# Kernel optimization log

Hardware: AMD Instinct MI355X
Metric: run time of the kernel (lower is better)

The kernel has to match this reference:

```python
import jax, jax.numpy as jnp
import numpy as np

D = 768

def setup_inputs() -> dict:
    key = jax.random.key(0)
    ks = jax.random.split(key, 12)
    inp = {
        "text_embeddings": jax.random.normal(ks[0], (8, 512, D), dtype=jnp.float32),
        "kb_emb": jax.random.normal(ks[1], (200000, D), dtype=jnp.float32),
        "W_ret": jax.random.normal(ks[2], (D, D), dtype=jnp.float32) * 0.02,
        "b_ret": jax.random.normal(ks[3], (D,), dtype=jnp.float32) * 0.02,
        "Ws1": jax.random.normal(ks[4], (2 * D, D), dtype=jnp.float32) * 0.02,
        "bs1": jax.random.normal(ks[5], (D,), dtype=jnp.float32) * 0.02,
        "Ws2": jax.random.normal(ks[6], (D, 1), dtype=jnp.float32) * 0.02,
        "bs2": jax.random.normal(ks[7], (1,), dtype=jnp.float32) * 0.02,
        "mention_sent": jax.random.randint(ks[8], (256,), 0, 8, dtype=jnp.int32),
        "mention_start": jax.random.randint(ks[9], (256,), 0, 480, dtype=jnp.int32),
        "mention_len": jax.random.randint(ks[10], (256,), 0, 31, dtype=jnp.int32),
        "top_k": 100,
    }
    return inp


def reference(text_embeddings, kb_emb, W_ret, b_ret, Ws1, bs1, Ws2, bs2,
              mention_sent, mention_start, mention_len, top_k):
    S = text_embeddings.shape[1]
    pos = jnp.arange(S, dtype=jnp.int32)
    # inclusive span [start, start+len] -> mask [M, S]
    mask = (pos[None, :] >= mention_start[:, None]) & (pos[None, :] <= (mention_start + mention_len)[:, None])
    maskf = mask.astype(text_embeddings.dtype)
    sent = text_embeddings[mention_sent]                       # [M, S, D]
    mention_emb = jnp.einsum('msd,ms->md', sent, maskf) / maskf.sum(1, keepdims=True)

    # entity_retriever linear, then KB dot-product retrieval of top 2k candidates
    query = mention_emb @ W_ret.T + b_ret                      # [M, D]
    sims = query @ kb_emb.T                                    # [M, N]
    _, cand_idx = jax.lax.top_k(sims, 2 * top_k)               # [M, 2k]
    cand_embs = kb_emb[cand_idx]                               # [M, 2k, D]

    # candidate_scorer: Linear(2D->D) on concat(mention, cand) + ReLU + Linear(D->1) + Sigmoid
    m_part = mention_emb @ Ws1[:D]                             # [M, D]
    c_part = jnp.einsum('mkd,de->mke', cand_embs, Ws1[D:])     # [M, 2k, D]
    h = jax.nn.relu(m_part[:, None, :] + c_part + bs1)
    scores = jax.nn.sigmoid(jnp.einsum('mke,eo->mko', h, Ws2)[..., 0] + bs2[0])  # [M, 2k]

    top_scores, ti = jax.lax.top_k(scores, top_k)              # [M, k]
    top_kb_idx = jnp.take_along_axis(cand_idx, ti, axis=1)
    return top_scores, top_kb_idx
```

## Files before the change

kernel.cpp:

```cpp
#include <hip/hip_runtime.h>
#include <cfloat>
#include <cmath>
#include <cstdint>

#define DD 768
#define MM 256
#define NKB 200000
#define SLEN 512
#define KK 200
#define TOPK 100
#define SURV_CAP 1024
#define RESC 232
#define THRC 2.70f
#define MAXMARK 32768
#define DELTA 4e-5
#define NET 12

typedef __attribute__((ext_vector_type(8))) short bf16x8;
typedef __attribute__((ext_vector_type(4))) float f32x4;

__device__ __forceinline__ unsigned short f2bf_rne(float x) {
  unsigned u = __float_as_uint(x);
  unsigned r = (u + 0x7FFFu + ((u >> 16) & 1u)) >> 16;
  return (unsigned short)r;
}
__device__ __forceinline__ float bf2f(unsigned short us) {
  return __uint_as_float(((unsigned)us) << 16);
}
__device__ __forceinline__ void splitbf(float x, unsigned short& hi, unsigned short& lo) {
  hi = f2bf_rne(x);
  lo = f2bf_rne(x - bf2f(hi));
}

__global__ __launch_bounds__(256) void k_prepT(
    const float* __restrict__ Wret, float* __restrict__ WretT) {
  __shared__ float tile[64][65];
  int e0 = blockIdx.x * 64, d0 = blockIdx.y * 64;
  int tid = threadIdx.x;
  int r = tid >> 6, cc = tid & 63;
  for (int i = 0; i < 64; i += 4)
    tile[r + i][cc] = Wret[(size_t)(e0 + r + i) * DD + d0 + cc];
  __syncthreads();
  for (int i = 0; i < 64; i += 4)
    WretT[(size_t)(d0 + r + i) * DD + e0 + cc] = tile[cc][r + i];
}

__global__ __launch_bounds__(256) void k_front(
    const float* __restrict__ text, const int* __restrict__ msent,
    const int* __restrict__ mstart, const int* __restrict__ mlen,
    const float* __restrict__ WretT, const float* __restrict__ bret,
    const float* __restrict__ Ws1,
    double* __restrict__ q64, unsigned short* __restrict__ qb16,
    float* __restrict__ tthr, double* __restrict__ mp64,
    float* __restrict__ mp32) {
  int m = blockIdx.x;
  __shared__ double sme[DD];
  __shared__ float snorm[256];
  int tid = threadIdx.x;
  {
    int sent = msent[m], st = mstart[m], ln = mlen[m];
    const float* base = text + (size_t)sent * SLEN * DD;
    for (int d = tid; d < DD; d += 256) {
      double acc = 0.0;
      for (int s = st; s <= st + ln; ++s) acc += (double)base[(size_t)s * DD + d];
      sme[d] = acc / (double)(ln + 1);
    }
  }
  __syncthreads();
  float nloc = 0.f;
  for (int e = tid; e < DD; e += 256) {
    double aq = (double)bret[e];
    double amp = 0.0;
    for (int d = 0; d < DD; ++d) {
      double md = sme[d];
      aq  += md * (double)WretT[(size_t)d * DD + e];
      amp += md * (double)Ws1[(size_t)d * DD + e];
    }
    q64[(size_t)m * DD + e] = aq;
    qb16[(size_t)m * DD + e] = f2bf_rne((float)aq);
    mp64[(size_t)m * DD + e] = amp;
    mp32[(size_t)m * DD + e] = (float)amp;
    nloc += (float)(aq * aq);
  }
  snorm[tid] = nloc; __syncthreads();
  for (int s = 128; s > 0; s >>= 1) {
    if (tid < s) snorm[tid] += snorm[tid + s];
    __syncthreads();
  }
  if (tid == 0) tthr[m] = THRC * sqrtf(snorm[0]);
}

__global__ __launch_bounds__(256) void k_prep(
    const float* __restrict__ Ws1, unsigned short* __restrict__ Bth,
    unsigned short* __restrict__ Btl) {
  int e = blockIdx.x;
  for (int k = threadIdx.x; k < DD; k += 256) {
    float x = Ws1[(size_t)(DD + k) * DD + e];
    unsigned short hi, lo;
    splitbf(x, hi, lo);
    Bth[(size_t)e * DD + k] = hi;
    Btl[(size_t)e * DD + k] = lo;
  }
}

__global__ __launch_bounds__(512) void k_sims_mfma(
    const unsigned short* __restrict__ qb, const float* __restrict__ kb,
    const float* __restrict__ tthr, int* __restrict__ gcnt,
    uint2* __restrict__ gcand) {
  __shared__ unsigned short Bs[64 * 32];
  __shared__ float sthr[256];
  int n0 = blockIdx.x * 64;
  int tid = threadIdx.x;
  int lane = tid & 63, w = tid >> 6;
  int h = lane >> 4, c = lane & 15;
  if (tid < 256) sthr[tid] = tthr[tid];
  f32x4 acc[2][4] = {};
  const int brow = n0 + (tid >> 3);
  const int bk4  = (tid & 7) * 4;
  const int bwoff = ((tid >> 3) * 64 + (tid & 7) * 8) ^ (((tid >> 3) & 7) << 4);
  auto ldB = [&](int k0, float4 &dst) {
    dst = *(const float4*)(kb + (size_t)brow * DD + k0 + bk4);
  };
  auto stB = [&](const float4 &v) {
    uint2 p;
    p.x = (unsigned)f2bf_rne(v.x) | ((unsigned)f2bf_rne(v.y) << 16);
    p.y = (unsigned)f2bf_rne(v.z) | ((unsigned)f2bf_rne(v.w) << 16);
    *(uint2*)((char*)Bs + bwoff) = p;
  };
  const unsigned short* qa0 = qb + (size_t)(w * 32 + c) * DD;
  const unsigned short* qa1 = qb + (size_t)(w * 32 + 16 + c) * DD;
  auto step = [&](int k0, float4 &cur, float4 &nxt, bool pf) {
    bf16x8 a0 = *(const bf16x8*)(qa0 + k0 + h * 8);
    bf16x8 a1 = *(const bf16x8*)(qa1 + k0 + h * 8);
    __syncthreads();
    stB(cur);
    if (pf) ldB(k0 + 32, nxt);
    __syncthreads();
#pragma unroll
    for (int nf = 0; nf < 4; ++nf) {
      int n = nf * 16 + c;
      int off = (n * 64 + h * 16) ^ ((n & 7) << 4);
      bf16x8 b = *(bf16x8*)((char*)Bs + off);
      acc[0][nf] = __builtin_amdgcn_mfma_f32_16x16x32_bf16(a0, b, acc[0][nf], 0, 0, 0);
      acc[1][nf] = __builtin_amdgcn_mfma_f32_16x16x32_bf16(a1, b, acc[1][nf], 0, 0, 0);
    }
  };
  float4 b0, b1;
  ldB(0, b0);
#pragma unroll
  for (int kc = 0; kc < 12; ++kc) {
    step(kc * 64,      b0, b1, true);
    step(kc * 64 + 32, b1, b0, kc < 11);
  }
#pragma unroll
  for (int mf = 0; mf < 2; ++mf)
#pragma unroll
    for (int nf = 0; nf < 4; ++nf)
#pragma unroll
      for (int r = 0; r < 4; ++r) {
        int row = w * 32 + mf * 16 + h * 4 + r;
        int col = n0 + nf * 16 + c;
        float v = acc[mf][nf][r];
        if (v > sthr[row]) {
          int p = atomicAdd(&gcnt[row], 1);
          if (p < SURV_CAP) gcand[(size_t)row * SURV_CAP + p] = make_uint2(__float_as_uint(v), (unsigned)col);
        }
      }
}

__global__ __launch_bounds__(256) void k_select(
    const uint2* __restrict__ gcand, const int* __restrict__ gcnt,
    const float* __restrict__ kb, const double* __restrict__ q64,
    int* __restrict__ cidx) {
  int m = blockIdx.x;
  __shared__ float skf[SURV_CAP];
  __shared__ int   sidx[SURV_CAP];
  __shared__ double sq[DD];
  __shared__ double skey[256];
  __shared__ int    skidx[256];
  int tid = threadIdx.x;
  int cnt = gcnt[m]; if (cnt > SURV_CAP) cnt = SURV_CAP;
  for (int d = tid; d < DD; d += 256) sq[d] = q64[(size_t)m * DD + d];
  for (int i = tid; i < SURV_CAP; i += 256) {
    if (i < cnt) {
      uint2 v = gcand[(size_t)m * SURV_CAP + i];
      skf[i] = __uint_as_float(v.x);
      sidx[i] = (int)v.y;
    } else { skf[i] = -FLT_MAX; sidx[i] = 0x7fffffff; }
  }
  __syncthreads();
  for (int k = 2; k <= SURV_CAP; k <<= 1) {
    for (int j = k >> 1; j > 0; j >>= 1) {
      for (int i = tid; i < SURV_CAP; i += 256) {
        int l = i ^ j;
        if (l > i) {
          float ka = skf[i], kb2 = skf[l];
          int ia = sidx[i], ib = sidx[l];
          bool lBefore = (kb2 > ka) || (kb2 == ka && ib < ia);
          bool iBefore = (ka > kb2) || (ka == kb2 && ia < ib);
          bool dir = ((i & k) == 0);
          bool sw = dir ? lBefore : iBefore;
          if (sw) { skf[i] = kb2; skf[l] = ka; sidx[i] = ib; sidx[l] = ia; }
        }
      }
      __syncthreads();
    }
  }
  int lane = tid & 63, wv = tid >> 6;
  for (int cpos = wv; cpos < RESC; cpos += 4) {
    int ci = sidx[cpos];
    double s;
    if (ci < NKB) {
      const float* krow = kb + (size_t)ci * DD;
      double acc = 0.0;
      for (int d = lane; d < DD; d += 64) acc += sq[d] * (double)krow[d];
      for (int off2 = 32; off2 > 0; off2 >>= 1) acc += __shfl_down(acc, off2, 64);
      s = acc;
    } else s = -INFINITY;
    if (lane == 0) { skey[cpos] = s; skidx[cpos] = ci; }
  }
  if (tid >= RESC && tid < 256) { skey[tid] = -INFINITY; skidx[tid] = 0x7fffffff; }
  __syncthreads();
  for (int k = 2; k <= 256; k <<= 1) {
    for (int j = k >> 1; j > 0; j >>= 1) {
      int i = tid, l = i ^ j;
      if (l > i) {
        double ka = skey[i], kb2 = skey[l];
        int ia = skidx[i], ib = skidx[l];
        bool lBefore = (kb2 > ka) || (kb2 == ka && ib < ia);
        bool iBefore = (ka > kb2) || (ka == kb2 && ia < ib);
        bool dir = ((i & k) == 0);
        bool sw = dir ? lBefore : iBefore;
        if (sw) { skey[i] = kb2; skey[l] = ka; skidx[i] = ib; skidx[l] = ia; }
      }
      __syncthreads();
    }
  }
  for (int cc = tid; cc < KK; cc += 256) {
    int v = skidx[cc];
    cidx[(size_t)m * KK + cc] = (v < NKB) ? v : 0;
  }
}

__global__ __launch_bounds__(256) void k_score2(
    const float* __restrict__ kb, const int* __restrict__ cidx,
    const float* __restrict__ mp32, const unsigned short* __restrict__ Bth,
    const unsigned short* __restrict__ Btl, const float* __restrict__ bs1,
    const float* __restrict__ Ws2, float* __restrict__ gpart) {
  __shared__ unsigned short Ah[256 * 32], Al[256 * 32];
  __shared__ unsigned short Bh[64 * 32], Bl[64 * 32];
  __shared__ float smp[3][64], sb1v[64], sw2v[64];
  __shared__ int srow[256];
  int p = blockIdx.x;
  int x = p & 7, j = p >> 3;
  int ct = x + 8 * (j / NET), et = j % NET;
  int r0 = ct * 256, e0 = et * 64;
  int tid = threadIdx.x, lane = tid & 63, w = tid >> 6;
  int h = lane >> 4, c = lane & 15;
  srow[tid] = cidx[r0 + tid];
  int m0 = r0 / KK;
  int mm1 = (m0 + 1 < MM) ? m0 + 1 : MM - 1;
  int mm2 = (m0 + 2 < MM) ? m0 + 2 : MM - 1;
  if (tid < 64) {
    smp[0][tid] = mp32[(size_t)m0 * DD + e0 + tid];
    smp[1][tid] = mp32[(size_t)mm1 * DD + e0 + tid];
    smp[2][tid] = mp32[(size_t)mm2 * DD + e0 + tid];
    sb1v[tid] = bs1[e0 + tid];
    sw2v[tid] = Ws2[e0 + tid];
  }
  __syncthreads();
  const float* aaddr[8];
#pragma unroll
  for (int it = 0; it < 8; ++it) {
    int idx = tid + it * 256;
    int rr = idx >> 3, f4 = idx & 7;
    aaddr[it] = kb + (size_t)srow[rr] * DD + f4 * 4;
  }
  const int be = tid >> 2, bk8 = tid & 3;
  const unsigned short* bhaddr = Bth + (size_t)(e0 + be) * DD + bk8 * 8;
  const unsigned short* bladdr = Btl + (size_t)(e0 + be) * DD + bk8 * 8;
  float4 pa[8];
  uint4 pbh, pbl;
#pragma unroll
  for (int it = 0; it < 8; ++it) pa[it] = *(const float4*)(aaddr[it]);
  pbh = *(const uint4*)(bhaddr);
  pbl = *(const uint4*)(bladdr);
  f32x4 acc[4][4] = {};
  for (int k0 = 0; k0 < DD; k0 += 32) {
    __syncthreads();
#pragma unroll
    for (int it = 0; it < 8; ++it) {
      int idx = tid + it * 256;
      int rr = idx >> 3, f4 = idx & 7;
      float4 v = pa[it];
      unsigned short h0, h1, h2, h3, l0, l1, l2, l3;
      splitbf(v.x, h0, l0); splitbf(v.y, h1, l1);
      splitbf(v.z, h2, l2); splitbf(v.w, h3, l3);
      uint2 ph, pl;
      ph.x = (unsigned)h0 | ((unsigned)h1 << 16); ph.y = (unsigned)h2 | ((unsigned)h3 << 16);
      pl.x = (unsigned)l0 | ((unsigned)l1 << 16); pl.y = (unsigned)l2 | ((unsigned)l3 << 16);
      int off = (rr * 64 + f4 * 8) ^ ((rr & 7) << 4);
      *(uint2*)((char*)Ah + off) = ph;
      *(uint2*)((char*)Al + off) = pl;
    }
    {
      int off = (be * 64 + bk8 * 16) ^ ((be & 7) << 4);
      *(uint4*)((char*)Bh + off) = pbh;
      *(uint4*)((char*)Bl + off) = pbl;
    }
    if (k0 + 32 < DD) {
#pragma unroll
      for (int it = 0; it < 8; ++it) pa[it] = *(const float4*)(aaddr[it] + k0 + 32);
      pbh = *(const uint4*)(bhaddr + k0 + 32);
      pbl = *(const uint4*)(bladdr + k0 + 32);
    }
    __syncthreads();
    bf16x8 ah[4], al[4];
#pragma unroll
    for (int mf = 0; mf < 4; ++mf) {
      int rr = w * 64 + mf * 16 + c;
      int off = (rr * 64 + h * 16) ^ ((rr & 7) << 4);
      ah[mf] = *(bf16x8*)((char*)Ah + off);
      al[mf] = *(bf16x8*)((char*)Al + off);
    }
#pragma unroll
    for (int nf = 0; nf < 4; ++nf) {
      int e = nf * 16 + c;
      int off = (e * 64 + h * 16) ^ ((e & 7) << 4);
      bf16x8 bh = *(bf16x8*)((char*)Bh + off);
      bf16x8 bl = *(bf16x8*)((char*)Bl + off);
#pragma unroll
      for (int mf = 0; mf < 4; ++mf) {
        acc[mf][nf] = __builtin_amdgcn_mfma_f32_16x16x32_bf16(ah[mf], bh, acc[mf][nf], 0, 0, 0);
        acc[mf][nf] = __builtin_amdgcn_mfma_f32_16x16x32_bf16(ah[mf], bl, acc[mf][nf], 0, 0, 0);
        acc[mf][nf] = __builtin_amdgcn_mfma_f32_16x16x32_bf16(al[mf], bh, acc[mf][nf], 0, 0, 0);
      }
    }
  }
  int bnd1 = (m0 + 1) * KK, bnd2 = (m0 + 2) * KK;
#pragma unroll
  for (int mf = 0; mf < 4; ++mf) {
    float zp[4] = {0.f, 0.f, 0.f, 0.f};
#pragma unroll
    for (int nf = 0; nf < 4; ++nf) {
      int el = nf * 16 + c;
      float b1v = sb1v[el], w2v = sw2v[el];
#pragma unroll
      for (int r = 0; r < 4; ++r) {
        int rowg = r0 + w * 64 + mf * 16 + h * 4 + r;
        int sel = (rowg >= bnd1) + (rowg >= bnd2);
        float hh = acc[mf][nf][r] + smp[sel][el] + b1v;
        if (hh > 0.f) zp[r] += hh * w2v;
      }
    }
#pragma unroll
    for (int r = 0; r < 4; ++r) {
      float v = zp[r];
      v += __shfl_xor(v, 1, 64);
      v += __shfl_xor(v, 2, 64);
      v += __shfl_xor(v, 4, 64);
      v += __shfl_xor(v, 8, 64);
      if (c == 0)
        gpart[(size_t)(r0 + w * 64 + mf * 16 + h * 4 + r) * NET + et] = v;
    }
  }
}

__global__ __launch_bounds__(256) void k_mark(
    const float* __restrict__ gpart, const float* __restrict__ bs2,
    double* __restrict__ z64, int* __restrict__ marks, int* __restrict__ mcnt) {
  int m = blockIdx.x;
  __shared__ double sk[256];
  __shared__ int sp[256];
  __shared__ int flag[256];
  int tid = threadIdx.x;
  flag[tid] = 0;
  if (tid < KK) {
    double s = 0.0;
#pragma unroll
    for (int i = 0; i < NET; ++i) s += (double)gpart[(size_t)(m * KK + tid) * NET + i];
    s += (double)bs2[0];
    z64[(size_t)m * KK + tid] = s;
    sk[tid] = s; sp[tid] = tid;
  } else { sk[tid] = -INFINITY; sp[tid] = 0x7fffffff; }
  __syncthreads();
  for (int k = 2; k <= 256; k <<= 1) {
    for (int j = k >> 1; j > 0; j >>= 1) {
      int i = tid, l = i ^ j;
      if (l > i) {
        double ka = sk[i], kb2 = sk[l];
        int ia = sp[i], ib = sp[l];
        bool lBefore = (kb2 > ka) || (kb2 == ka && ib < ia);
        bool iBefore = (ka > kb2) || (ka == kb2 && ia < ib);
        bool dir = ((i & k) == 0);
        bool sw = dir ? lBefore : iBefore;
        if (sw) { sk[i] = kb2; sk[l] = ka; sp[i] = ib; sp[l] = ia; }
      }
      __syncthreads();
    }
  }
  if (tid <= 120) {
    if (sk[tid] - sk[tid + 1] < DELTA) {
      flag[tid] = 1;
      atomicExch(&flag[tid + 1], 1);
    }
  }
  __syncthreads();
  if (tid <= 121 && flag[tid]) {
    int p = atomicAdd(mcnt, 1);
    if (p < MAXMARK) marks[p] = m * KK + sp[tid];
  }
}

__global__ __launch_bounds__(256) void k_rescore(
    const float* __restrict__ kb, const int* __restrict__ cidx,
    const double* __restrict__ mp64, const float* __restrict__ Ws1,
    const float* __restrict__ bs1, const float* __restrict__ Ws2,
    const float* __restrict__ bs2, const int* __restrict__ marks,
    const int* __restrict__ mcnt, double* __restrict__ z64) {
  int cnt = *mcnt; if (cnt > MAXMARK) cnt = MAXMARK;
  __shared__ float sc[DD];
  __shared__ double sred[256];
  int tid = threadIdx.x;
  for (int it = blockIdx.x; it < cnt; it += gridDim.x) {
    int r = marks[it];
    int m = r / KK;
    int row = cidx[r];
    for (int d = tid; d < DD; d += 256) sc[d] = kb[(size_t)row * DD + d];
    __syncthreads();
    double pz = 0.0;
    for (int e = tid; e < DD; e += 256) {
      double a = 0.0;
      for (int d = 0; d < DD; ++d) a += (double)sc[d] * (double)Ws1[(size_t)(DD + d) * DD + e];
      double hv = mp64[(size_t)m * DD + e] + a + (double)bs1[e];
      if (hv > 0) pz += hv * (double)Ws2[e];
    }
    sred[tid] = pz; __syncthreads();
    for (int s = 128; s > 0; s >>= 1) { if (tid < s) sred[tid] += sred[tid + s]; __syncthreads(); }
    if (tid == 0) z64[r] = sred[0] + (double)bs2[0];
    __syncthreads();
  }
}

__global__ __launch_bounds__(256) void k_final(
    const double* __restrict__ z64, const int* __restrict__ cidx, float* __restrict__ out) {
  int m = blockIdx.x;
  __shared__ double sk[256];
  __shared__ int sp[256];
  int tid = threadIdx.x;
  if (tid < KK) { sk[tid] = z64[(size_t)m * KK + tid]; sp[tid] = tid; }
  else { sk[tid] = -INFINITY; sp[tid] = 0x7fffffff; }
  __syncthreads();
  for (int k = 2; k <= 256; k <<= 1) {
    for (int j = k >> 1; j > 0; j >>= 1) {
      int i = tid, l = i ^ j;
      if (l > i) {
        double ka = sk[i], kb2 = sk[l];
        int ia = sp[i], ib = sp[l];
        bool lBefore = (kb2 > ka) || (kb2 == ka && ib < ia);
        bool iBefore = (ka > kb2) || (ka == kb2 && ia < ib);
        bool dir = ((i & k) == 0);
        bool sw = dir ? lBefore : iBefore;
        if (sw) { sk[i] = kb2; sk[l] = ka; sp[i] = ib; sp[l] = ia; }
      }
      __syncthreads();
    }
  }
  if (tid < TOPK) {
    double z = sk[tid];
    out[(size_t)m * TOPK + tid] = (float)(1.0 / (1.0 + exp(-z)));
    out[(size_t)MM * TOPK + (size_t)m * TOPK + tid] = (float)cidx[(size_t)m * KK + sp[tid]];
  }
}

extern "C" void kernel_launch(void* const* d_in, const int* in_sizes, int n_in,
                              void* d_out, int out_size, void* d_ws, size_t ws_size,
                              hipStream_t stream) {
  const float* text  = (const float*)d_in[0];
  const float* kb    = (const float*)d_in[1];
  const float* Wret  = (const float*)d_in[2];
  const float* bret  = (const float*)d_in[3];
  const float* Ws1   = (const float*)d_in[4];
  const float* bs1   = (const float*)d_in[5];
  const float* Ws2   = (const float*)d_in[6];
  const float* bs2   = (const float*)d_in[7];
  const int* msent   = (const int*)d_in[8];
  const int* mstart  = (const int*)d_in[9];
  const int* mlen    = (const int*)d_in[10];
  float* out = (float*)d_out;

  char* ws = (char*)d_ws;
  size_t off = 0;
  auto alloc = [&](size_t bytes) -> void* {
    void* p = ws + off;
    off = (off + bytes + 255) & ~(size_t)255;
    return p;
  };
  double* q64  = (double*)alloc((size_t)MM * DD * 8);
  unsigned short* qb16 = (unsigned short*)alloc((size_t)MM * DD * 2);
  float*  tthr = (float*) alloc((size_t)MM * 4);
  double* mp64 = (double*)alloc((size_t)MM * DD * 8);
  float*  mp32 = (float*) alloc((size_t)MM * DD * 4);
  int*    cidx = (int*)   alloc((size_t)MM * KK * 4);
  double* z64  = (double*)alloc((size_t)MM * KK * 8);
  float*  gpart = (float*)alloc((size_t)MM * KK * NET * 4);
  int*    marks = (int*)  alloc((size_t)MAXMARK * 4);
  int*    mcnt  = (int*)  alloc(256);
  int*    gcnt  = (int*)  alloc((size_t)MM * 4);
  uint2*  gcand = (uint2*)alloc((size_t)MM * SURV_CAP * 8);
  unsigned short* Bth = (unsigned short*)alloc((size_t)DD * DD * 2);
  unsigned short* Btl = (unsigned short*)alloc((size_t)DD * DD * 2);
  float*  WretT = (float*)alloc((size_t)DD * DD * 4);
  (void)ws_size;

  dim3 gt(DD / 64, DD / 64);
  k_prepT<<<gt, 256, 0, stream>>>(Wret, WretT);
  k_prep<<<DD, 256, 0, stream>>>(Ws1, Bth, Btl);
  k_front<<<MM, 256, 0, stream>>>(text, msent, mstart, mlen, WretT, bret, Ws1,
                                  q64, qb16, tthr, mp64, mp32);

  hipMemsetAsync(gcnt, 0, (size_t)MM * 4, stream);
  k_sims_mfma<<<NKB / 64, 512, 0, stream>>>(qb16, kb, tthr, gcnt, gcand);
  k_select<<<MM, 256, 0, stream>>>(gcand, gcnt, kb, q64, cidx);

  k_score2<<<(MM * KK / 256) * NET, 256, 0, stream>>>(kb, cidx, mp32, Bth, Btl, bs1, Ws2, gpart);
  hipMemsetAsync(mcnt, 0, 4, stream);
  k_mark<<<MM, 256, 0, stream>>>(gpart, bs2, z64, marks, mcnt);
  k_rescore<<<2048, 256, 0, stream>>>(kb, cidx, mp64, Ws1, bs1, Ws2, bs2, marks, mcnt, z64);
  k_final<<<MM, 256, 0, stream>>>(z64, cidx, out);
}
```

Measured before the change: 1.305 ms.

## Double-buffer LDS in sims GEMM and pre-split candidate rows to bf16 hi/lo

The KB similarity kernel now uses two LDS buffers with a three-stage register prefetch. This cuts the barriers per k-step from two to one and overlaps global loads with MFMA work. Separately, a new pre-pass kernel gathers each candidate embedding once and splits it into bf16 hi/lo arrays. The scorer then loads those directly, so the split is no longer repeated in each of the 12 e-tiles. This costs an extra kernel launch and about 157 MB of workspace writes and reads.

```diff
diff --git a/kernel.cpp b/kernel.cpp
--- a/kernel.cpp
+++ b/kernel.cpp
@@ -107,7 +107,7 @@
     const unsigned short* __restrict__ qb, const float* __restrict__ kb,
     const float* __restrict__ tthr, int* __restrict__ gcnt,
     uint2* __restrict__ gcand) {
-  __shared__ unsigned short Bs[64 * 32];
+  __shared__ unsigned short Bs[2][64 * 32];
   __shared__ float sthr[256];
   int n0 = blockIdx.x * 64;
   int tid = threadIdx.x;
@@ -118,39 +118,42 @@
   const int brow = n0 + (tid >> 3);
   const int bk4  = (tid & 7) * 4;
   const int bwoff = ((tid >> 3) * 64 + (tid & 7) * 8) ^ (((tid >> 3) & 7) << 4);
-  auto ldB = [&](int k0, float4 &dst) {
-    dst = *(const float4*)(kb + (size_t)brow * DD + k0 + bk4);
+  auto ldB = [&](int k0) -> float4 {
+    return *(const float4*)(kb + (size_t)brow * DD + k0 + bk4);
   };
-  auto stB = [&](const float4 &v) {
+  auto stB = [&](int buf, const float4 &v) {
     uint2 p;
     p.x = (unsigned)f2bf_rne(v.x) | ((unsigned)f2bf_rne(v.y) << 16);
     p.y = (unsigned)f2bf_rne(v.z) | ((unsigned)f2bf_rne(v.w) << 16);
-    *(uint2*)((char*)Bs + bwoff) = p;
+    *(uint2*)((char*)Bs + buf * 4096 + bwoff) = p;
   };
   const unsigned short* qa0 = qb + (size_t)(w * 32 + c) * DD;
   const unsigned short* qa1 = qb + (size_t)(w * 32 + 16 + c) * DD;
-  auto step = [&](int k0, float4 &cur, float4 &nxt, bool pf) {
-    bf16x8 a0 = *(const bf16x8*)(qa0 + k0 + h * 8);
-    bf16x8 a1 = *(const bf16x8*)(qa1 + k0 + h * 8);
-    __syncthreads();
-    stB(cur);
-    if (pf) ldB(k0 + 32, nxt);
-    __syncthreads();
+  stB(0, ldB(0));
+  float4 pend1 = ldB(32);
+  float4 pend2 = ldB(64);
+  bf16x8 a0 = *(const bf16x8*)(qa0 + h * 8);
+  bf16x8 a1 = *(const bf16x8*)(qa1 + h * 8);
+  __syncthreads();
+#pragma unroll
+  for (int s = 0; s < 24; ++s) {
+    int cur = s & 1;
+    if (s + 1 < 24) stB(cur ^ 1, pend1);
+    pend1 = pend2;
+    if (s + 3 < 24) pend2 = ldB((s + 3) * 32);
+    int kn = (s + 1 < 24) ? (s + 1) * 32 : s * 32;
+    bf16x8 a0n = *(const bf16x8*)(qa0 + kn + h * 8);
+    bf16x8 a1n = *(const bf16x8*)(qa1 + kn + h * 8);
 #pragma unroll
     for (int nf = 0; nf < 4; ++nf) {
       int n = nf * 16 + c;
       int off = (n * 64 + h * 16) ^ ((n & 7) << 4);
-      bf16x8 b = *(bf16x8*)((char*)Bs + off);
+      bf16x8 b = *(bf16x8*)((char*)Bs + cur * 4096 + off);
       acc[0][nf] = __builtin_amdgcn_mfma_f32_16x16x32_bf16(a0, b, acc[0][nf], 0, 0, 0);
       acc[1][nf] = __builtin_amdgcn_mfma_f32_16x16x32_bf16(a1, b, acc[1][nf], 0, 0, 0);
     }
-  };
-  float4 b0, b1;
-  ldB(0, b0);
-#pragma unroll
-  for (int kc = 0; kc < 12; ++kc) {
-    step(kc * 64,      b0, b1, true);
-    step(kc * 64 + 32, b1, b0, kc < 11);
+    a0 = a0n; a1 = a1n;
+    __syncthreads();
   }
 #pragma unroll
   for (int mf = 0; mf < 2; ++mf)
@@ -242,22 +245,43 @@
   }
 }
 
+__global__ __launch_bounds__(256) void k_presplit(
+    const float* __restrict__ kb, const int* __restrict__ cidx,
+    unsigned short* __restrict__ Ahg, unsigned short* __restrict__ Alg) {
+  int base = blockIdx.x * 8;
+  int tid = threadIdx.x;
+  int lr = tid >> 5, t = tid & 31;
+  int row = cidx[base + lr];
+  const float* src = kb + (size_t)row * DD;
+  unsigned short* dh = Ahg + (size_t)(base + lr) * DD;
+  unsigned short* dl = Alg + (size_t)(base + lr) * DD;
+  for (int i = t; i < DD / 4; i += 32) {
+    float4 v = *(const float4*)(src + i * 4);
+    unsigned short h0, h1, h2, h3, l0, l1, l2, l3;
+    splitbf(v.x, h0, l0); splitbf(v.y, h1, l1);
+    splitbf(v.z, h2, l2); splitbf(v.w, h3, l3);
+    uint2 ph, pl;
+    ph.x = (unsigned)h0 | ((unsigned)h1 << 16); ph.y = (unsigned)h2 | ((unsigned)h3 << 16);
+    pl.x = (unsigned)l0 | ((unsigned)l1 << 16); pl.y = (unsigned)l2 | ((unsigned)l3 << 16);
+    *(uint2*)(dh + i * 4) = ph;
+    *(uint2*)(dl + i * 4) = pl;
+  }
+}
+
 __global__ __launch_bounds__(256) void k_score2(
-    const float* __restrict__ kb, const int* __restrict__ cidx,
+    const unsigned short* __restrict__ Ahg, const unsigned short* __restrict__ Alg,
     const float* __restrict__ mp32, const unsigned short* __restrict__ Bth,
     const unsigned short* __restrict__ Btl, const float* __restrict__ bs1,
     const float* __restrict__ Ws2, float* __restrict__ gpart) {
   __shared__ unsigned short Ah[256 * 32], Al[256 * 32];
   __shared__ unsigned short Bh[64 * 32], Bl[64 * 32];
   __shared__ float smp[3][64], sb1v[64], sw2v[64];
-  __shared__ int srow[256];
   int p = blockIdx.x;
   int x = p & 7, j = p >> 3;
   int ct = x + 8 * (j / NET), et = j % NET;
   int r0 = ct * 256, e0 = et * 64;
   int tid = threadIdx.x, lane = tid & 63, w = tid >> 6;
   int h = lane >> 4, c = lane & 15;
-  srow[tid] = cidx[r0 + tid];
   int m0 = r0 / KK;
   int mm1 = (m0 + 1 < MM) ? m0 + 1 : MM - 1;
   int mm2 = (m0 + 2 < MM) ? m0 + 2 : MM - 1;
@@ -268,40 +292,36 @@
     sb1v[tid] = bs1[e0 + tid];
     sw2v[tid] = Ws2[e0 + tid];
   }
-  __syncthreads();
-  const float* aaddr[8];
-#pragma unroll
-  for (int it = 0; it < 8; ++it) {
+  const unsigned short* ahaddr[4];
+  const unsigned short* aladdr[4];
+#pragma unroll
+  for (int it = 0; it < 4; ++it) {
     int idx = tid + it * 256;
-    int rr = idx >> 3, f4 = idx & 7;
-    aaddr[it] = kb + (size_t)srow[rr] * DD + f4 * 4;
+    int rr = idx >> 2, k8 = idx & 3;
+    ahaddr[it] = Ahg + (size_t)(r0 + rr) * DD + k8 * 8;
+    aladdr[it] = Alg + (size_t)(r0 + rr) * DD + k8 * 8;
   }
   const int be = tid >> 2, bk8 = tid & 3;
   const unsigned short* bhaddr = Bth + (size_t)(e0 + be) * DD + bk8 * 8;
   const unsigned short* bladdr = Btl + (size_t)(e0 + be) * DD + bk8 * 8;
-  float4 pa[8];
-  uint4 pbh, pbl;
-#pragma unroll
-  for (int it = 0; it < 8; ++it) pa[it] = *(const float4*)(aaddr[it]);
+  uint4 pah[4], pal[4], pbh, pbl;
+#pragma unroll
+  for (int it = 0; it < 4; ++it) {
+    pah[it] = *(const uint4*)(ahaddr[it]);
+    pal[it] = *(const uint4*)(aladdr[it]);
+  }
   pbh = *(const uint4*)(bhaddr);
   pbl = *(const uint4*)(bladdr);
   f32x4 acc[4][4] = {};
   for (int k0 = 0; k0 < DD; k0 += 32) {
     __syncthreads();
 #pragma unroll
-    for (int it = 0; it < 8; ++it) {
+    for (int it = 0; it < 4; ++it) {
       int idx = tid + it * 256;
-      int rr = idx >> 3, f4 = idx & 7;
-      float4 v = pa[it];
-      unsigned short h0, h1, h2, h3, l0, l1, l2, l3;
-      splitbf(v.x, h0, l0); splitbf(v.y, h1, l1);
-      splitbf(v.z, h2, l2); splitbf(v.w, h3, l3);
-      uint2 ph, pl;
-      ph.x = (unsigned)h0 | ((unsigned)h1 << 16); ph.y = (unsigned)h2 | ((unsigned)h3 << 16);
-      pl.x = (unsigned)l0 | ((unsigned)l1 << 16); pl.y = (unsigned)l2 | ((unsigned)l3 << 16);
-      int off = (rr * 64 + f4 * 8) ^ ((rr & 7) << 4);
-      *(uint2*)((char*)Ah + off) = ph;
-      *(uint2*)((char*)Al + off) = pl;
+      int rr = idx >> 2, k8 = idx & 3;
+      int off = (rr * 64 + k8 * 16) ^ ((rr & 7) << 4);
+      *(uint4*)((char*)Ah + off) = pah[it];
+      *(uint4*)((char*)Al + off) = pal[it];
     }
     {
       int off = (be * 64 + bk8 * 16) ^ ((be & 7) << 4);
@@ -310,7 +330,10 @@
     }
     if (k0 + 32 < DD) {
 #pragma unroll
-      for (int it = 0; it < 8; ++it) pa[it] = *(const float4*)(aaddr[it] + k0 + 32);
+      for (int it = 0; it < 4; ++it) {
+        pah[it] = *(const uint4*)(ahaddr[it] + k0 + 32);
+        pal[it] = *(const uint4*)(aladdr[it] + k0 + 32);
+      }
       pbh = *(const uint4*)(bhaddr + k0 + 32);
       pbl = *(const uint4*)(bladdr + k0 + 32);
     }
@@ -511,6 +534,8 @@
   unsigned short* Bth = (unsigned short*)alloc((size_t)DD * DD * 2);
   unsigned short* Btl = (unsigned short*)alloc((size_t)DD * DD * 2);
   float*  WretT = (float*)alloc((size_t)DD * DD * 4);
+  unsigned short* Ahg = (unsigned short*)alloc((size_t)MM * KK * DD * 2);
+  unsigned short* Alg = (unsigned short*)alloc((size_t)MM * KK * DD * 2);
   (void)ws_size;
 
   dim3 gt(DD / 64, DD / 64);
@@ -523,7 +548,8 @@
   k_sims_mfma<<<NKB / 64, 512, 0, stream>>>(qb16, kb, tthr, gcnt, gcand);
   k_select<<<MM, 256, 0, stream>>>(gcand, gcnt, kb, q64, cidx);
 
-  k_score2<<<(MM * KK / 256) * NET, 256, 0, stream>>>(kb, cidx, mp32, Bth, Btl, bs1, Ws2, gpart);
+  k_presplit<<<(MM * KK) / 8, 256, 0, stream>>>(kb, cidx, Ahg, Alg);
+  k_score2<<<(MM * KK / 256) * NET, 256, 0, stream>>>(Ahg, Alg, mp32, Bth, Btl, bs1, Ws2, gpart);
   hipMemsetAsync(mcnt, 0, 4, stream);
   k_mark<<<MM, 256, 0, stream>>>(gpart, bs2, z64, marks, mcnt);
   k_rescore<<<2048, 256, 0, stream>>>(kb, cidx, mp64, Ws1, bs1, Ws2, bs2, marks, mcnt, z64);
```

Measured after the change: 1.761 ms. 34.9% more time.

## Double-buffer KB tile in LDS with deeper prefetch in sims kernel

Applied to the files above, without the earlier changes.

Reworks the sims MFMA main loop to use two LDS buffers for the bf16-converted KB tile, so each step needs one barrier instead of two. Global loads of KB rows are now issued two steps ahead, and the query A fragments for the next step are loaded early. The aim is to hide global memory latency and cut synchronization overhead in this bandwidth-bound scan over the 200k-row KB. In exchange it doubles LDS use and raises register pressure from the extra in-flight float4 and bf16 fragments, which could lower occupancy.

```diff
diff --git a/kernel.cpp b/kernel.cpp
--- a/kernel.cpp
+++ b/kernel.cpp
@@ -107,7 +107,7 @@
     const unsigned short* __restrict__ qb, const float* __restrict__ kb,
     const float* __restrict__ tthr, int* __restrict__ gcnt,
     uint2* __restrict__ gcand) {
-  __shared__ unsigned short Bs[64 * 32];
+  __shared__ unsigned short Bs[2][64 * 32];
   __shared__ float sthr[256];
   int n0 = blockIdx.x * 64;
   int tid = threadIdx.x;
@@ -118,39 +118,42 @@
   const int brow = n0 + (tid >> 3);
   const int bk4  = (tid & 7) * 4;
   const int bwoff = ((tid >> 3) * 64 + (tid & 7) * 8) ^ (((tid >> 3) & 7) << 4);
-  auto ldB = [&](int k0, float4 &dst) {
-    dst = *(const float4*)(kb + (size_t)brow * DD + k0 + bk4);
+  auto ldB = [&](int k0) -> float4 {
+    return *(const float4*)(kb + (size_t)brow * DD + k0 + bk4);
   };
-  auto stB = [&](const float4 &v) {
+  auto stB = [&](int buf, const float4 &v) {
     uint2 p;
     p.x = (unsigned)f2bf_rne(v.x) | ((unsigned)f2bf_rne(v.y) << 16);
     p.y = (unsigned)f2bf_rne(v.z) | ((unsigned)f2bf_rne(v.w) << 16);
-    *(uint2*)((char*)Bs + bwoff) = p;
+    *(uint2*)((char*)Bs + buf * 4096 + bwoff) = p;
   };
   const unsigned short* qa0 = qb + (size_t)(w * 32 + c) * DD;
   const unsigned short* qa1 = qb + (size_t)(w * 32 + 16 + c) * DD;
-  auto step = [&](int k0, float4 &cur, float4 &nxt, bool pf) {
-    bf16x8 a0 = *(const bf16x8*)(qa0 + k0 + h * 8);
-    bf16x8 a1 = *(const bf16x8*)(qa1 + k0 + h * 8);
-    __syncthreads();
-    stB(cur);
-    if (pf) ldB(k0 + 32, nxt);
-    __syncthreads();
+  stB(0, ldB(0));
+  float4 pend1 = ldB(32);
+  float4 pend2 = ldB(64);
+  bf16x8 a0 = *(const bf16x8*)(qa0 + h * 8);
+  bf16x8 a1 = *(const bf16x8*)(qa1 + h * 8);
+  __syncthreads();
+#pragma unroll
+  for (int s = 0; s < 24; ++s) {
+    int cur = s & 1;
+    if (s + 1 < 24) stB(cur ^ 1, pend1);
+    pend1 = pend2;
+    if (s + 3 < 24) pend2 = ldB((s + 3) * 32);
+    int kn = (s + 1 < 24) ? (s + 1) * 32 : s * 32;
+    bf16x8 a0n = *(const bf16x8*)(qa0 + kn + h * 8);
+    bf16x8 a1n = *(const bf16x8*)(qa1 + kn + h * 8);
 #pragma unroll
     for (int nf = 0; nf < 4; ++nf) {
       int n = nf * 16 + c;
       int off = (n * 64 + h * 16) ^ ((n & 7) << 4);
-      bf16x8 b = *(bf16x8*)((char*)Bs + off);
+      bf16x8 b = *(bf16x8*)((char*)Bs + cur * 4096 + off);
       acc[0][nf] = __builtin_amdgcn_mfma_f32_16x16x32_bf16(a0, b, acc[0][nf], 0, 0, 0);
       acc[1][nf] = __builtin_amdgcn_mfma_f32_16x16x32_bf16(a1, b, acc[1][nf], 0, 0, 0);
     }
-  };
-  float4 b0, b1;
-  ldB(0, b0);
-#pragma unroll
-  for (int kc = 0; kc < 12; ++kc) {
-    step(kc * 64,      b0, b1, true);
-    step(kc * 64 + 32, b1, b0, kc < 11);
+    a0 = a0n; a1 = a1n;
+    __syncthreads();
   }
 #pragma unroll
   for (int mf = 0; mf < 2; ++mf)
```

Result: no change. 1.307 ms (+0.1%).

## Double-buffer KB tile in LDS with deeper register prefetch in sims kernel

Applied to the files above, without the earlier changes.

The sims MFMA kernel now stages 64-wide K chunks of KB rows into two alternating LDS buffers. It keeps two chunks of global loads in flight in registers and drops one of the two barriers per step. The goal is to hide the latency of streaming the large KB from HBM behind MFMA work and to cut synchronisation count. The cost is more LDS and more live registers per thread, which could lower occupancy.

```diff
diff --git a/kernel.cpp b/kernel.cpp
--- a/kernel.cpp
+++ b/kernel.cpp
@@ -107,7 +107,7 @@
     const unsigned short* __restrict__ qb, const float* __restrict__ kb,
     const float* __restrict__ tthr, int* __restrict__ gcnt,
     uint2* __restrict__ gcand) {
-  __shared__ unsigned short Bs[64 * 32];
+  __shared__ unsigned short Bs[2][64 * 64];
   __shared__ float sthr[256];
   int n0 = blockIdx.x * 64;
   int tid = threadIdx.x;
@@ -116,41 +116,57 @@
   if (tid < 256) sthr[tid] = tthr[tid];
   f32x4 acc[2][4] = {};
   const int brow = n0 + (tid >> 3);
-  const int bk4  = (tid & 7) * 4;
-  const int bwoff = ((tid >> 3) * 64 + (tid & 7) * 8) ^ (((tid >> 3) & 7) << 4);
-  auto ldB = [&](int k0, float4 &dst) {
-    dst = *(const float4*)(kb + (size_t)brow * DD + k0 + bk4);
+  const int bg   = tid & 7;
+  const int bwoff = ((tid >> 3) * 128 + bg * 16) ^ (((tid >> 3) & 7) << 4);
+  auto ldB = [&](int k0, float4 &d0, float4 &d1) {
+    const float* s = kb + (size_t)brow * DD + k0 + bg * 8;
+    d0 = *(const float4*)(s);
+    d1 = *(const float4*)(s + 4);
   };
-  auto stB = [&](const float4 &v) {
-    uint2 p;
-    p.x = (unsigned)f2bf_rne(v.x) | ((unsigned)f2bf_rne(v.y) << 16);
-    p.y = (unsigned)f2bf_rne(v.z) | ((unsigned)f2bf_rne(v.w) << 16);
-    *(uint2*)((char*)Bs + bwoff) = p;
+  auto stB = [&](int buf, const float4 &v0, const float4 &v1) {
+    uint4 p;
+    p.x = (unsigned)f2bf_rne(v0.x) | ((unsigned)f2bf_rne(v0.y) << 16);
+    p.y = (unsigned)f2bf_rne(v0.z) | ((unsigned)f2bf_rne(v0.w) << 16);
+    p.z = (unsigned)f2bf_rne(v1.x) | ((unsigned)f2bf_rne(v1.y) << 16);
+    p.w = (unsigned)f2bf_rne(v1.z) | ((unsigned)f2bf_rne(v1.w) << 16);
+    *(uint4*)((char*)Bs + buf * 8192 + bwoff) = p;
   };
   const unsigned short* qa0 = qb + (size_t)(w * 32 + c) * DD;
   const unsigned short* qa1 = qb + (size_t)(w * 32 + 16 + c) * DD;
-  auto step = [&](int k0, float4 &cur, float4 &nxt, bool pf) {
-    bf16x8 a0 = *(const bf16x8*)(qa0 + k0 + h * 8);
-    bf16x8 a1 = *(const bf16x8*)(qa1 + k0 + h * 8);
-    __syncthreads();
-    stB(cur);
-    if (pf) ldB(k0 + 32, nxt);
-    __syncthreads();
+  float4 c0, c1, p1a, p1b, p2a, p2b;
+  ldB(0, c0, c1);
+  stB(0, c0, c1);
+  ldB(64, p1a, p1b);
+  ldB(128, p2a, p2b);
+  __syncthreads();
+#pragma unroll
+  for (int s = 0; s < 12; ++s) {
+    int cur = s & 1;
+    int k0 = s * 64;
+    if (s + 1 < 12) stB(cur ^ 1, p1a, p1b);
+    p1a = p2a; p1b = p2b;
+    if (s + 3 < 12) ldB((s + 3) * 64, p2a, p2b);
+    bf16x8 a00 = *(const bf16x8*)(qa0 + k0 + h * 8);
+    bf16x8 a10 = *(const bf16x8*)(qa1 + k0 + h * 8);
+    bf16x8 a01 = *(const bf16x8*)(qa0 + k0 + 32 + h * 8);
+    bf16x8 a11 = *(const bf16x8*)(qa1 + k0 + 32 + h * 8);
 #pragma unroll
     for (int nf = 0; nf < 4; ++nf) {
       int n = nf * 16 + c;
-      int off = (n * 64 + h * 16) ^ ((n & 7) << 4);
-      bf16x8 b = *(bf16x8*)((char*)Bs + off);
-      acc[0][nf] = __builtin_amdgcn_mfma_f32_16x16x32_bf16(a0, b, acc[0][nf], 0, 0, 0);
-      acc[1][nf] = __builtin_amdgcn_mfma_f32_16x16x32_bf16(a1, b, acc[1][nf], 0, 0, 0);
-    }
-  };
-  float4 b0, b1;
-  ldB(0, b0);
-#pragma unroll
-  for (int kc = 0; kc < 12; ++kc) {
-    step(kc * 64,      b0, b1, true);
-    step(kc * 64 + 32, b1, b0, kc < 11);
+      int off = (n * 128 + h * 16) ^ ((n & 7) << 4);
+      bf16x8 b = *(bf16x8*)((char*)Bs + cur * 8192 + off);
+      acc[0][nf] = __builtin_amdgcn_mfma_f32_16x16x32_bf16(a00, b, acc[0][nf], 0, 0, 0);
+      acc[1][nf] = __builtin_amdgcn_mfma_f32_16x16x32_bf16(a10, b, acc[1][nf], 0, 0, 0);
+    }
+#pragma unroll
+    for (int nf = 0; nf < 4; ++nf) {
+      int n = nf * 16 + c;
+      int off = (n * 128 + 64 + h * 16) ^ ((n & 7) << 4);
+      bf16x8 b = *(bf16x8*)((char*)Bs + cur * 8192 + off);
+      acc[0][nf] = __builtin_amdgcn_mfma_f32_16x16x32_bf16(a01, b, acc[0][nf], 0, 0, 0);
+      acc[1][nf] = __builtin_amdgcn_mfma_f32_16x16x32_bf16(a11, b, acc[1][nf], 0, 0, 0);
+    }
+    __syncthreads();
   }
 #pragma unroll
   for (int mf = 0; mf < 2; ++mf)
```

Result: no change. 1.287 ms (median of 2 runs) (-1.4%).
